# Kernel optimization log

Hardware: AMD Instinct MI355X
Metric: run time of the kernel (lower is better)

## Reference

```python
import jax, jax.numpy as jnp
import numpy as np

H_DIM = 512
FF_DIM = 2048
N_HEAD = 4
N_BLOCK = 3
N_TOKEN = 128
B, S = 8, 1024
LN_EPS = 1e-5


def _layernorm(x, g, b):
    mu = jnp.mean(x, axis=-1, keepdims=True)
    var = jnp.mean(jnp.square(x - mu), axis=-1, keepdims=True)
    return (x - mu) * jax.lax.rsqrt(var + LN_EPS) * g + b


def setup_inputs() -> dict:
    key = jax.random.key(0)
    ks = jax.random.split(key, 20)
    sc = 0.02
    inp = {
        'input_ids': jax.random.randint(ks[0], (B, S), 0, N_TOKEN, dtype=jnp.int32),
        'attention_mask': jnp.ones((B, S), dtype=jnp.int32),
        'emb': jax.random.uniform(ks[1], (N_TOKEN, H_DIM), dtype=jnp.float32),
        'wq': jax.random.normal(ks[2], (N_BLOCK, N_HEAD, H_DIM, H_DIM), dtype=jnp.float32) * sc,
        'wk': jax.random.normal(ks[3], (N_BLOCK, N_HEAD, H_DIM, H_DIM), dtype=jnp.float32) * sc,
        'wv': jax.random.normal(ks[4], (N_BLOCK, N_HEAD, H_DIM, H_DIM), dtype=jnp.float32) * sc,
        'wo_w': jax.random.normal(ks[5], (N_BLOCK, N_HEAD * H_DIM, H_DIM), dtype=jnp.float32) * sc,
        'wo_b': jnp.zeros((N_BLOCK, H_DIM), dtype=jnp.float32),
        'ln1_g': jnp.ones((N_BLOCK, H_DIM), dtype=jnp.float32),
        'ln1_b': jnp.zeros((N_BLOCK, H_DIM), dtype=jnp.float32),
        'ff1_w': jax.random.normal(ks[6], (N_BLOCK, FF_DIM, H_DIM), dtype=jnp.float32) * sc,
        'ff1_b': jnp.zeros((N_BLOCK, FF_DIM), dtype=jnp.float32),
        'ff2_w': jax.random.normal(ks[7], (N_BLOCK, H_DIM, FF_DIM), dtype=jnp.float32) * sc,
        'ff2_b': jnp.zeros((N_BLOCK, H_DIM), dtype=jnp.float32),
        'ln2_g': jnp.ones((N_BLOCK, H_DIM), dtype=jnp.float32),
        'ln2_b': jnp.zeros((N_BLOCK, H_DIM), dtype=jnp.float32),
        'lm_w': jax.random.normal(ks[8], (H_DIM, N_TOKEN), dtype=jnp.float32) * sc,
    }
    return inp


def reference(emb, wq, wk, wv, wo_w, wo_b, ln1_g, ln1_b, ff1_w, ff1_b,
              ff2_w, ff2_b, ln2_g, ln2_b, lm_w, input_ids, attention_mask):
    mask_f = attention_mask.astype(jnp.float32)          # [B,S]
    valid = attention_mask != 0                          # [B,S]

    # Embedding lookup
    x = emb[input_ids]                                   # [B,S,H]

    # Positional encoding: positions assigned sequentially to valid tokens;
    # both even and odd feature slots get the SAME sin value (per source).
    pos = jnp.cumsum(mask_f, axis=-1) - 1.0              # [B,S]
    div = jnp.exp(jnp.arange(0, H_DIM, 2, dtype=jnp.float32) * (-jnp.log(10000.0) / H_DIM))  # [H/2]
    s = jnp.sin(pos[..., None] * div)                    # [B,S,H/2]
    pos_enc = jnp.repeat(s, 2, axis=-1) * mask_f[..., None]
    x = x + pos_enc

    # Allowed attention: causal (key <= query) AND query valid AND key valid
    rows = jnp.arange(S)
    causal = rows[None, :, None] >= rows[None, None, :]  # [1,S,S] (query>=key)
    allowed = causal & valid[:, :, None] & valid[:, None, :]  # [B,S,S]
    neg_inf = jnp.float32(-jnp.inf)
    scale = jnp.sqrt(jnp.float32(H_DIM))

    for l in range(N_BLOCK):
        # Per-head full-width attention (each head uses full H_DIM)
        q = jnp.einsum('bsh,nhd->bnsd', x, wq[l])
        k = jnp.einsum('bsh,nhd->bnsd', x, wk[l])
        v = jnp.einsum('bsh,nhd->bnsd', x, wv[l])
        scores = jnp.einsum('bnsd,bntd->bnst', q, k) / scale      # [B,N,S,S]
        scores = jnp.where(allowed[:, None], scores, neg_inf)
        att = jax.nn.softmax(scores, axis=-1)
        att = jnp.where(jnp.isnan(att), 0.0, att)                  # NaN rows -> 0
        o = jnp.einsum('bnst,bntd->bnsd', att, v)                  # [B,N,S,H]
        o = jnp.transpose(o, (0, 2, 1, 3)).reshape(B, S, N_HEAD * H_DIM)
        mh = o @ wo_w[l] + wo_b[l]
        x = _layernorm(x + mh, ln1_g[l], ln1_b[l])
        # Conv1d with kernel 1 == pointwise linear
        ff = jax.nn.relu(jnp.einsum('bsh,fh->bsf', x, ff1_w[l]) + ff1_b[l])
        ff = jnp.einsum('bsf,hf->bsh', ff, ff2_w[l]) + ff2_b[l]
        x = _layernorm(x + ff, ln2_g[l], ln2_b[l])

    return x @ lm_w                                       # [B,S,N_TOKEN]
```

## Files before the change

### kernel.cpp

```cpp
#include <hip/hip_runtime.h>
#include <hip/hip_bf16.h>

#define S_LEN 1024
#define BATCH 8
#define HD 512
#define FFD 2048
#define NHEAD 4
#define NBLK 3
#define NTOK 128

typedef __bf16 bf16_t;
typedef __bf16 bf16x4_t __attribute__((ext_vector_type(4)));
typedef __bf16 bf16x8_t __attribute__((ext_vector_type(8)));
typedef float f32x4_t __attribute__((ext_vector_type(4)));

typedef __attribute__((address_space(3))) uint32_t lds_u32;
typedef __attribute__((address_space(1))) uint32_t glb_u32;

template<int NI>
__device__ __forceinline__ void ldsread(const bf16_t* __restrict__ buf, int row0,
                                        int fr, int fg, int sw, bf16x8_t (&dst)[NI][2]) {
  #pragma unroll
  for (int i = 0; i < NI; ++i)
    #pragma unroll
    for (int ks = 0; ks < 2; ++ks)
      dst[i][ks] = *(const bf16x8_t*)&buf[(row0 + i*16 + fr)*64 + (((ks*4 + fg) ^ sw) << 3)];
}

template<int IB, int JB>
__device__ __forceinline__ void mquad(f32x4_t (&acc)[8][4],
                                      const bf16x8_t (&af)[4][2], const bf16x8_t (&bf)[2][2]) {
  #pragma unroll
  for (int ks = 0; ks < 2; ++ks)
    #pragma unroll
    for (int i = 0; i < 4; ++i)
      #pragma unroll
      for (int j = 0; j < 2; ++j)
        acc[IB+i][JB+j] = __builtin_amdgcn_mfma_f32_16x16x32_bf16(af[i][ks], bf[j][ks], acc[IB+i][JB+j], 0, 0, 0);
}

template<bool OUT_BF16, bool BIAS, bool RELU, bool TRI, bool CKLIM>
__global__ __launch_bounds__(512, 2)
void gemm256_kernel(const bf16_t* __restrict__ A,
                    const bf16_t* __restrict__ Bt,
                    const float* __restrict__ bias,
                    void* __restrict__ Cv,
                    int M, int N, int K,
                    int lda, int ldb, int ldc,
                    long long sA, long long sB, int bshift, long long sBias,
                    int zshift, long long sC_hi, long long sC_lo,
                    int msub_shift, long long msub_stride,
                    float alpha)
{
  const int zb = blockIdx.z;
  int m0, n0;
  if (TRI) {
    const int idx = blockIdx.x;
    int mi = (int)((sqrtf(8.f * idx + 1.f) - 1.f) * 0.5f);
    while ((mi + 1) * (mi + 2) / 2 <= idx) ++mi;
    while (mi * (mi + 1) / 2 > idx) --mi;
    m0 = mi * 256;
    n0 = (idx - mi * (mi + 1) / 2) * 256;
  } else {
    m0 = blockIdx.x * 256;
    n0 = blockIdx.y * 256;
  }
  int kend = K;
  if (CKLIM) { int ke = m0 + 256; kend = ke < K ? ke : K; }
  const int nt = kend >> 6;

  const bf16_t* Az = A + (long long)zb * sA;
  const bf16_t* Bz = Bt + (long long)(zb >> bshift) * sB;
  const long long coff = ((long long)(zb >> zshift)) * sC_hi
                       + ((long long)(zb & ((1 << zshift) - 1))) * sC_lo;

  __shared__ __align__(16) bf16_t As[2][256 * 64];
  __shared__ __align__(16) bf16_t Bs[2][256 * 64];

  const int tid = threadIdx.x;
  const int lane = tid & 63;
  const int w = tid >> 6;
  const int wm = (w >> 2) * 128;
  const int wn = (w & 3) * 64;
  const int fr = lane & 15;
  const int fg = lane >> 4;
  const int sw = fr & 7;

  const int srow = tid >> 3;
  const int scol8 = tid & 7;
  const int gswz = ((scol8 ^ (srow & 7)) << 3);

  f32x4_t acc[8][4];
  #pragma unroll
  for (int i = 0; i < 8; ++i)
    #pragma unroll
    for (int j = 0; j < 4; ++j)
      acc[i][j] = (f32x4_t){0.f, 0.f, 0.f, 0.f};

  const bf16_t* gA0 = Az + (long long)(m0 + srow) * lda + gswz;
  const bf16_t* gB0 = Bz + (long long)(n0 + srow) * ldb + gswz;

  auto stage_half = [&](int buf, int kt, int h) {
    if (h < 2) {
      const bf16_t* g = gA0 + (long long)(h * 128) * lda + (kt << 6);
      bf16_t* l = &As[buf][(h*128 + srow) * 64 + (scol8 << 3)];
      __builtin_amdgcn_global_load_lds((const glb_u32*)g, (lds_u32*)l, 16, 0, 0);
      __builtin_amdgcn_global_load_lds((const glb_u32*)(g + 64LL*lda), (lds_u32*)(l + 64*64), 16, 0, 0);
    } else {
      const int hh = h - 2;
      const bf16_t* g = gB0 + (long long)(hh * 128) * ldb + (kt << 6);
      bf16_t* l = &Bs[buf][(hh*128 + srow) * 64 + (scol8 << 3)];
      __builtin_amdgcn_global_load_lds((const glb_u32*)g, (lds_u32*)l, 16, 0, 0);
      __builtin_amdgcn_global_load_lds((const glb_u32*)(g + 64LL*ldb), (lds_u32*)(l + 64*64), 16, 0, 0);
    }
  };

  stage_half(0, 0, 0); stage_half(0, 0, 1); stage_half(0, 0, 2); stage_half(0, 0, 3);
  if (nt > 1) { stage_half(1, 1, 0); stage_half(1, 1, 1); }
  if (nt > 1) asm volatile("s_waitcnt vmcnt(4)" ::: "memory");
  else        asm volatile("s_waitcnt vmcnt(0)" ::: "memory");
  __builtin_amdgcn_s_barrier();
  __builtin_amdgcn_sched_barrier(0);

  for (int t = 0; t < nt; ++t) {
    const int cur = t & 1;
    const bf16_t* Ac = &As[cur][0];
    const bf16_t* Bc = &Bs[cur][0];
    bf16x8_t a0[4][2], a1[4][2], b0[2][2], b1[2][2];

    ldsread<4>(Ac, wm, fr, fg, sw, a0);
    ldsread<2>(Bc, wn, fr, fg, sw, b0);
    if (t + 1 < nt) stage_half(cur ^ 1, t + 1, 2);
    mquad<0, 0>(acc, a0, b0);
    ldsread<4>(Ac, wm + 64, fr, fg, sw, a1);
    ldsread<2>(Bc, wn + 32, fr, fg, sw, b1);
    if (t + 1 < nt) stage_half(cur ^ 1, t + 1, 3);
    mquad<4, 2>(acc, a1, b1);

    __builtin_amdgcn_s_barrier();
    __builtin_amdgcn_sched_barrier(0);

    if (t + 2 < nt) stage_half(cur, t + 2, 0);
    mquad<0, 2>(acc, a0, b1);
    if (t + 2 < nt) {
      stage_half(cur, t + 2, 1);
      asm volatile("s_waitcnt vmcnt(4)" ::: "memory");
    } else {
      asm volatile("s_waitcnt vmcnt(0)" ::: "memory");
    }
    mquad<4, 0>(acc, a1, b0);

    __builtin_amdgcn_s_barrier();
    __builtin_amdgcn_sched_barrier(0);
  }

  #pragma unroll
  for (int i = 0; i < 8; ++i) {
    #pragma unroll
    for (int e = 0; e < 4; ++e) {
      const int row = m0 + wm + i*16 + fg*4 + e;
      const long long ro = coff
        + ((long long)(row >> msub_shift)) * msub_stride
        + (long long)(row & ((1 << msub_shift) - 1)) * (long long)ldc;
      #pragma unroll
      for (int j = 0; j < 4; ++j) {
        const int col = n0 + wn + j*16 + fr;
        float v = acc[i][j][e] * alpha;
        if (BIAS) v += bias[(long long)zb * sBias + col];
        if (RELU) v = v > 0.f ? v : 0.f;
        if (OUT_BF16) ((bf16_t*)Cv)[ro + col] = (bf16_t)v;
        else          ((float*)Cv)[ro + col]  = v;
      }
    }
  }
}

template<bool OUT_BF16, bool BIAS, bool RELU, bool CSKIP, bool CKLIM>
__global__ __launch_bounds__(256, 2)
void gemm_bt_kernel(const bf16_t* __restrict__ A,
                    const bf16_t* __restrict__ Bt,
                    const float* __restrict__ bias,
                    void* __restrict__ Cv,
                    int M, int N, int K,
                    int lda, int ldb, int ldc,
                    long long sA, long long sB, long long sBias,
                    int zshift, long long sC_hi, long long sC_lo,
                    int msub_shift, long long msub_stride,
                    float alpha)
{
  const int zb = blockIdx.z;
  const int m0 = blockIdx.x * 128;
  const int n0 = blockIdx.y * 128;
  if (CSKIP && n0 > m0 + 127) return;
  int kend = K;
  if (CKLIM) { int ke = m0 + 128; kend = ke < K ? ke : K; }

  const bf16_t* Az = A + (long long)zb * sA;
  const bf16_t* Bz = Bt + (long long)zb * sB;
  const long long coff = ((long long)(zb >> zshift)) * sC_hi
                       + ((long long)(zb & ((1 << zshift) - 1))) * sC_lo;

  __shared__ __align__(16) bf16_t As[128 * 64];
  __shared__ __align__(16) bf16_t Bs[128 * 64];

  const int tid = threadIdx.x;
  const int wv = tid >> 6;
  const int lane = tid & 63;
  const int wm = (wv >> 1) * 64;
  const int wn = (wv & 1) * 64;
  const int fr = lane & 15;
  const int fg = lane >> 4;
  const int sw = fr & 7;

  f32x4_t acc[4][4];
  #pragma unroll
  for (int i = 0; i < 4; ++i)
    #pragma unroll
    for (int j = 0; j < 4; ++j)
      acc[i][j] = (f32x4_t){0.f, 0.f, 0.f, 0.f};

  const bf16_t* ga = Az + (long long)(m0 + (wv << 5) + (lane >> 3)) * lda
                   + (((lane & 7) ^ (lane >> 3)) << 3);
  const bf16_t* gb = Bz + (long long)(n0 + (wv << 5) + (lane >> 3)) * ldb
                   + (((lane & 7) ^ (lane >> 3)) << 3);

  for (int k0 = 0; k0 < kend; k0 += 64) {
    #pragma unroll
    for (int s = 0; s < 4; ++s) {
      __builtin_amdgcn_global_load_lds(
        (const glb_u32*)(ga + (long long)s * 8 * lda + k0),
        (lds_u32*)(As + (wv * 4 + s) * 512), 16, 0, 0);
      __builtin_amdgcn_global_load_lds(
        (const glb_u32*)(gb + (long long)s * 8 * ldb + k0),
        (lds_u32*)(Bs + (wv * 4 + s) * 512), 16, 0, 0);
    }
    __syncthreads();
    #pragma unroll
    for (int kc = 0; kc < 2; ++kc) {
      const int ca = ((kc * 4 + fg) ^ sw) << 3;
      bf16x8_t af[4], bfr[4];
      #pragma unroll
      for (int i = 0; i < 4; ++i)
        af[i] = *(const bf16x8_t*)&As[(wm + i*16 + fr) * 64 + ca];
      #pragma unroll
      for (int j = 0; j < 4; ++j)
        bfr[j] = *(const bf16x8_t*)&Bs[(wn + j*16 + fr) * 64 + ca];
      #pragma unroll
      for (int i = 0; i < 4; ++i)
        #pragma unroll
        for (int j = 0; j < 4; ++j)
          acc[i][j] = __builtin_amdgcn_mfma_f32_16x16x32_bf16(af[i], bfr[j], acc[i][j], 0, 0, 0);
    }
    __syncthreads();
  }

  #pragma unroll
  for (int i = 0; i < 4; ++i) {
    #pragma unroll
    for (int e = 0; e < 4; ++e) {
      const int row = m0 + wm + i*16 + fg*4 + e;
      const long long ro = coff
        + ((long long)(row >> msub_shift)) * msub_stride
        + (long long)(row & ((1 << msub_shift) - 1)) * (long long)ldc;
      #pragma unroll
      for (int j = 0; j < 4; ++j) {
        const int col = n0 + wn + j*16 + fr;
        float v = acc[i][j][e] * alpha;
        if (BIAS) v += bias[(long long)zb * sBias + col];
        if (RELU) v = v > 0.f ? v : 0.f;
        if (OUT_BF16) ((bf16_t*)Cv)[ro + col] = (bf16_t)v;
        else          ((float*)Cv)[ro + col]  = v;
      }
    }
  }
}

template<typename TIN>
__global__ void transpose_kernel(const TIN* __restrict__ in, bf16_t* __restrict__ out,
                                 int R, int C, long long sIn, long long sOut)
{
  __shared__ float tile[32][33];
  const long long zi = (long long)blockIdx.z * sIn;
  const long long zo = (long long)blockIdx.z * sOut;
  const int c0 = blockIdx.x * 32, r0 = blockIdx.y * 32;
  const int tx = threadIdx.x, ty = threadIdx.y;
  #pragma unroll
  for (int i = 0; i < 4; ++i) {
    int r = r0 + ty + i*8;
    tile[ty + i*8][tx] = (float)in[zi + (long long)r * C + c0 + tx];
  }
  __syncthreads();
  #pragma unroll
  for (int i = 0; i < 4; ++i) {
    int c = c0 + ty + i*8;
    out[zo + (long long)c * R + r0 + tx] = (bf16_t)tile[tx][ty + i*8];
  }
}

__global__ void convert2_kernel(const float* __restrict__ a, const float* __restrict__ b,
                                bf16_t* __restrict__ out, long long n)
{
  long long i = (long long)blockIdx.x * blockDim.x + threadIdx.x;
  long long stride = (long long)gridDim.x * blockDim.x;
  for (; i < 2*n; i += stride)
    out[i] = (bf16_t)(i < n ? a[i] : b[i - n]);
}

__global__ void fill_kernel(float* __restrict__ out, long long n, float v)
{
  long long i = (long long)blockIdx.x * blockDim.x + threadIdx.x;
  long long stride = (long long)gridDim.x * blockDim.x;
  for (; i < n; i += stride) out[i] = v;
}

__global__ void pos_kernel(const int* __restrict__ mask, float* __restrict__ pos)
{
  __shared__ float scn[S_LEN];
  const int b = blockIdx.x, t = threadIdx.x;
  scn[t] = (float)(mask[b * S_LEN + t] != 0);
  __syncthreads();
  for (int off = 1; off < S_LEN; off <<= 1) {
    float add = (t >= off) ? scn[t - off] : 0.f;
    __syncthreads();
    scn[t] += add;
    __syncthreads();
  }
  pos[b * S_LEN + t] = scn[t] - 1.0f;
}

__global__ void embed_kernel(const int* __restrict__ ids, const int* __restrict__ mask,
                             const float* __restrict__ pos, const float* __restrict__ emb,
                             float* __restrict__ x, bf16_t* __restrict__ xb)
{
  const int idx = blockIdx.x * 256 + threadIdx.x;
  const int i = idx & 255;
  const int bs = idx >> 8;
  const int id = ids[bs];
  const float m = (float)(mask[bs] != 0);
  const float p = pos[bs];
  const float dv = __expf(-(float)(2 * i) * (9.210340371976184f / (float)HD));
  const float sv = __sinf(p * dv) * m;
  const float e0 = emb[id * HD + 2*i], e1 = emb[id * HD + 2*i + 1];
  const float x0 = e0 + sv, x1 = e1 + sv;
  x[(long long)bs * HD + 2*i]     = x0;
  x[(long long)bs * HD + 2*i + 1] = x1;
  xb[(long long)bs * HD + 2*i]     = (bf16_t)x0;
  xb[(long long)bs * HD + 2*i + 1] = (bf16_t)x1;
}

__global__ void softmax_kernel(bf16_t* __restrict__ scP,
                               const int* __restrict__ mask, int pair0)
{
  const int lane = threadIdx.x & 63;
  const int s = blockIdx.x * 4 + (threadIdx.x >> 6);
  const int pz = blockIdx.y;
  const int b = (pair0 + pz) >> 2;
  bf16_t* row = scP + ((long long)pz * S_LEN + s) * S_LEN;
  const int t0 = lane * 16;

  bf16x8_t r0 = *(const bf16x8_t*)&row[t0];
  bf16x8_t r1 = *(const bf16x8_t*)&row[t0 + 8];
  int4 m4[4];
  #pragma unroll
  for (int q = 0; q < 4; ++q) m4[q] = *(const int4*)&mask[b * S_LEN + t0 + q*4];
  const int* mm = (const int*)m4;

  float v[16]; bool ok[16];
  #pragma unroll
  for (int j = 0; j < 16; ++j) {
    const int t = t0 + j;
    ok[j] = (t <= s) && (mm[j] != 0);
    float raw = (j < 8) ? (float)r0[j] : (float)r1[j - 8];
    v[j] = ok[j] ? raw : -INFINITY;
  }
  float mx = v[0];
  #pragma unroll
  for (int j = 1; j < 16; ++j) mx = fmaxf(mx, v[j]);
  #pragma unroll
  for (int o = 32; o; o >>= 1) mx = fmaxf(mx, __shfl_xor(mx, o));

  float e[16]; float sum = 0.f;
  #pragma unroll
  for (int j = 0; j < 16; ++j) { e[j] = ok[j] ? __expf(v[j] - mx) : 0.f; sum += e[j]; }
  #pragma unroll
  for (int o = 32; o; o >>= 1) sum += __shfl_xor(sum, o);

  const bool qvalid = mask[b * S_LEN + s] != 0;
  const float inv = (qvalid && sum > 0.f) ? 1.f / sum : 0.f;
  bf16x8_t o0, o1;
  #pragma unroll
  for (int j = 0; j < 8; ++j) { o0[j] = (bf16_t)(e[j] * inv); o1[j] = (bf16_t)(e[j+8] * inv); }
  *(bf16x8_t*)&row[t0] = o0;
  *(bf16x8_t*)&row[t0 + 8] = o1;
}

__global__ void ln_kernel(float* __restrict__ x, const float* __restrict__ tparts,
                          int ns, long long pstride,
                          const float* __restrict__ bias,
                          const float* __restrict__ g, const float* __restrict__ b,
                          bf16_t* __restrict__ xb)
{
  const int lane = threadIdx.x & 63;
  const long long row = (long long)blockIdx.x * 4 + (threadIdx.x >> 6);
  const int e0 = lane * 8;
  const long long base = row * HD + e0;

  float4 xa = *(const float4*)&x[base];
  float4 xc = *(const float4*)&x[base + 4];
  float4 ba = *(const float4*)&bias[e0];
  float4 bc = *(const float4*)&bias[e0 + 4];
  float v[8] = {xa.x+ba.x, xa.y+ba.y, xa.z+ba.z, xa.w+ba.w,
                xc.x+bc.x, xc.y+bc.y, xc.z+bc.z, xc.w+bc.w};
  for (int i = 0; i < ns; ++i) {
    float4 p0 = *(const float4*)&tparts[i*pstride + base];
    float4 p1 = *(const float4*)&tparts[i*pstride + base + 4];
    v[0]+=p0.x; v[1]+=p0.y; v[2]+=p0.z; v[3]+=p0.w;
    v[4]+=p1.x; v[5]+=p1.y; v[6]+=p1.z; v[7]+=p1.w;
  }
  float s = 0.f;
  #pragma unroll
  for (int j = 0; j < 8; ++j) s += v[j];
  #pragma unroll
  for (int o = 32; o; o >>= 1) s += __shfl_xor(s, o);
  const float mu = s * (1.f / (float)HD);
  float q = 0.f;
  #pragma unroll
  for (int j = 0; j < 8; ++j) { v[j] -= mu; q += v[j]*v[j]; }
  #pragma unroll
  for (int o = 32; o; o >>= 1) q += __shfl_xor(q, o);
  const float inv = rsqrtf(q * (1.f / (float)HD) + 1e-5f);

  float4 ga4 = *(const float4*)&g[e0];
  float4 gc4 = *(const float4*)&g[e0 + 4];
  float4 bb4 = *(const float4*)&b[e0];
  float4 bd4 = *(const float4*)&b[e0 + 4];
  float y[8] = {v[0]*inv*ga4.x+bb4.x, v[1]*inv*ga4.y+bb4.y, v[2]*inv*ga4.z+bb4.z, v[3]*inv*ga4.w+bb4.w,
                v[4]*inv*gc4.x+bd4.x, v[5]*inv*gc4.y+bd4.y, v[6]*inv*gc4.z+bd4.z, v[7]*inv*gc4.w+bd4.w};
  *(float4*)&x[base]     = (float4){y[0],y[1],y[2],y[3]};
  *(float4*)&x[base + 4] = (float4){y[4],y[5],y[6],y[7]};
  bf16x8_t yb;
  #pragma unroll
  for (int j = 0; j < 8; ++j) yb[j] = (bf16_t)y[j];
  *(bf16x8_t*)&xb[base] = yb;
}

extern "C" void kernel_launch(void* const* d_in, const int* in_sizes, int n_in,
                              void* d_out, int out_size, void* d_ws, size_t ws_size,
                              hipStream_t stream)
{
  (void)in_sizes; (void)n_in;
  const int*   ids   = (const int*)d_in[0];
  const int*   amask = (const int*)d_in[1];
  const float* emb   = (const float*)d_in[2];
  const float* wq    = (const float*)d_in[3];
  const float* wk    = (const float*)d_in[4];
  const float* wv    = (const float*)d_in[5];
  const float* wo_w  = (const float*)d_in[6];
  const float* wo_b  = (const float*)d_in[7];
  const float* ln1_g = (const float*)d_in[8];
  const float* ln1_b = (const float*)d_in[9];
  const float* ff1_w = (const float*)d_in[10];
  const float* ff1_b = (const float*)d_in[11];
  const float* ff2_w = (const float*)d_in[12];
  const float* ff2_b = (const float*)d_in[13];
  const float* ln2_g = (const float*)d_in[14];
  const float* ln2_b = (const float*)d_in[15];
  const float* lm_w  = (const float*)d_in[16];

  const long long MROW = (long long)BATCH * S_LEN;
  const size_t MBc = 1ull << 20;
  char* p = (char*)d_ws;
  auto alloc = [&](size_t bytes) { char* r = p; p += (bytes + 255) & ~(size_t)255; return r; };

  float*  x     = (float*) alloc(MROW * HD * 4);
  bf16_t* xb    = (bf16_t*)alloc(MROW * HD * 2);
  bf16_t* ob    = (bf16_t*)alloc(MROW * (NHEAD*HD) * 2);
  bf16_t* wqkb  = (bf16_t*)alloc(8LL * HD * HD * 2);
  bf16_t* wvT   = (bf16_t*)alloc(4LL * HD * HD * 2);
  bf16_t* Gt    = (bf16_t*)alloc(4LL * HD * HD * 2);
  bf16_t* woT   = (bf16_t*)alloc((long long)HD * FFD * 2);
  bf16_t* wff1  = (bf16_t*)alloc((long long)FFD * HD * 2);
  bf16_t* wff2  = (bf16_t*)alloc((long long)HD * FFD * 2);
  bf16_t* lmT   = (bf16_t*)alloc((long long)NTOK * HD * 2);
  float*  pos   = (float*) alloc(MROW * 4);

  const size_t used = (size_t)(p - (char*)d_ws);
  const size_t rem  = ws_size > used ? ws_size - used : 0;

  int P = 0, SK = 2;
  if      (rem >= 128 * MBc) { P = 32; SK = 4; }
  else if (rem >= 64 * MBc)  { P = 8;  SK = 2; }
  if (P == 0) {
    fill_kernel<<<1024, 256, 0, stream>>>((float*)d_out, (long long)out_size,
                                          (float)(ws_size >> 20));
    return;
  }

  char* A = p;
  const long long pairE = (long long)S_LEN * HD;
  bf16_t* qc  = (bf16_t*)A;
  bf16_t* vTc = qc  + (long long)P * pairE;
  bf16_t* scb = vTc + (long long)P * pairE;
  float*  tmp = (float*)A;
  bf16_t* ffb = (bf16_t*)(A + (size_t)SK * 16 * MBc);

  const dim3 tb(32, 8);
  transpose_kernel<float><<<dim3(4,16,1), tb, 0, stream>>>(lm_w, lmT, HD, NTOK, 0, 0);
  pos_kernel<<<BATCH, S_LEN, 0, stream>>>(amask, pos);
  embed_kernel<<<8192, 256, 0, stream>>>(ids, amask, pos, emb, x, xb);

  const int nch = 32 / P;
  const int bpc = P / NHEAD;

  for (int l = 0; l < NBLK; ++l) {
    convert2_kernel<<<2048, 256, 0, stream>>>(
      wq + (long long)l*NHEAD*HD*HD, wk + (long long)l*NHEAD*HD*HD, wqkb, 4LL*HD*HD);
    transpose_kernel<float><<<dim3(16,16,4), tb, 0, stream>>>(
      wv + (long long)l*NHEAD*HD*HD, wvT, HD, HD, (long long)HD*HD, (long long)HD*HD);
    transpose_kernel<float><<<dim3(16,64,1), tb, 0, stream>>>(
      wo_w + (long long)l*FFD*HD, woT, FFD, HD, 0, 0);
    convert2_kernel<<<2048, 256, 0, stream>>>(
      ff1_w + (long long)l*FFD*HD, ff2_w + (long long)l*HD*FFD, wff1, (long long)FFD*HD);
    gemm_bt_kernel<true,false,false,false,false><<<dim3(4,4,4),256,0,stream>>>(
      wqkb + 4LL*HD*HD, wqkb, nullptr, Gt,
      HD, HD, HD, HD, HD, HD,
      (long long)HD*HD, (long long)HD*HD, 0,
      30, 0, (long long)HD*HD,
      30, 0, 1.f);

    for (int c = 0; c < nch; ++c) {
      const int b0 = c * bpc;
      const int pair0 = b0 * NHEAD;
      const int Mch = bpc * S_LEN;

      gemm256_kernel<true,false,false,false,false><<<dim3(Mch/256,2,4),512,0,stream>>>(
        xb + (long long)b0*S_LEN*HD, Gt, nullptr, qc, Mch, HD, HD, HD, HD, HD,
        0, (long long)HD*HD, 0, 0,
        2, 0, pairE,
        10, (long long)NHEAD*pairE, 1.f);

      gemm256_kernel<true,false,false,false,false><<<dim3(8,4,bpc),512,0,stream>>>(
        wvT, xb + (long long)b0*S_LEN*HD, nullptr, vTc,
        2048, S_LEN, HD, HD, HD, S_LEN,
        0, (long long)S_LEN*HD, 0, 0,
        0, (long long)NHEAD*HD*S_LEN, 0,
        9, (long long)HD*S_LEN, 1.f);

      gemm256_kernel<true,false,false,true,false><<<dim3(10,1,P),512,0,stream>>>(
        qc, xb + (long long)b0*S_LEN*HD, nullptr, scb,
        S_LEN, S_LEN, HD, HD, HD, S_LEN,
        pairE, (long long)S_LEN*HD, 2, 0,
        30, 0, (long long)S_LEN*S_LEN,
        30, 0, 0.044194173824159216f);
      softmax_kernel<<<dim3(S_LEN/4,P),256,0,stream>>>(scb, amask, pair0);
      gemm_bt_kernel<true,false,false,false,true><<<dim3(8,4,P),256,0,stream>>>(
        scb, vTc, nullptr,
        ob + (long long)b0*S_LEN*(NHEAD*HD),
        S_LEN, HD, S_LEN, S_LEN, S_LEN, NHEAD*HD,
        (long long)S_LEN*S_LEN, (long long)HD*S_LEN, 0,
        2, (long long)S_LEN*NHEAD*HD, HD,
        30, 0, 1.f);
    }

    gemm256_kernel<false,false,false,false,false><<<dim3(32,2,SK),512,0,stream>>>(
      ob, woT, nullptr, tmp,
      (int)MROW, HD, (NHEAD*HD)/SK, NHEAD*HD, NHEAD*HD, HD,
      (NHEAD*HD)/SK, (NHEAD*HD)/SK, 0, 0,
      0, (long long)MROW*HD, 0,
      30, 0, 1.f);
    ln_kernel<<<2048,256,0,stream>>>(x, tmp, SK, (long long)MROW*HD,
                                     wo_b + l*HD, ln1_g + l*HD, ln1_b + l*HD, xb);

    gemm256_kernel<true,true,true,false,false><<<dim3(32,8,1),512,0,stream>>>(
      xb, wff1, ff1_b + l*FFD, ffb,
      (int)MROW, FFD, HD, HD, HD, FFD,
      0, 0, 0, 0, 30, 0, 0, 30, 0, 1.f);
    gemm256_kernel<false,false,false,false,false><<<dim3(32,2,SK),512,0,stream>>>(
      ffb, wff2, nullptr, tmp,
      (int)MROW, HD, FFD/SK, FFD, FFD, HD,
      FFD/SK, FFD/SK, 0, 0,
      0, (long long)MROW*HD, 0,
      30, 0, 1.f);
    ln_kernel<<<2048,256,0,stream>>>(x, tmp, SK, (long long)MROW*HD,
                                     ff2_b + l*HD, ln2_g + l*HD, ln2_b + l*HD, xb);
  }

  gemm_bt_kernel<false,false,false,false,false><<<dim3(64,1,1),256,0,stream>>>(
    xb, lmT, nullptr, (float*)d_out,
    (int)MROW, NTOK, HD, HD, HD, NTOK,
    0, 0, 0, 30, 0, 0, 30, 0, 1.f);
}
```

Measured before the change: 902.4 us.

## Fuse softmax exponentiation into score GEMM and defer normalization to PV GEMM

Drops the separate softmax kernel. The score GEMM epilogue now applies the causal and key masks, exponentiates the scaled scores without subtracting the row max, and writes unnormalized bf16 probabilities. It also reduces partial row sums into LDS and writes them per column tile. A small kernel combines the partial sums into reciprocal row norms, and the PV GEMM multiplies its output by them. The score GEMM also switches to single-buffered LDS to free shared memory, which removes load/compute overlap, and skipping the max subtraction risks overflow if scores grow large.

```diff
diff --git a/kernel.cpp b/kernel.cpp
--- a/kernel.cpp
+++ b/kernel.cpp
@@ -39,7 +39,7 @@
         acc[IB+i][JB+j] = __builtin_amdgcn_mfma_f32_16x16x32_bf16(af[i][ks], bf[j][ks], acc[IB+i][JB+j], 0, 0, 0);
 }
 
-template<bool OUT_BF16, bool BIAS, bool RELU, bool TRI, bool CKLIM>
+template<bool OUT_BF16, bool BIAS, bool RELU, bool TRI, bool CKLIM, bool SB, bool SM>
 __global__ __launch_bounds__(512, 2)
 void gemm256_kernel(const bf16_t* __restrict__ A,
                     const bf16_t* __restrict__ Bt,
@@ -50,17 +50,19 @@
                     long long sA, long long sB, int bshift, long long sBias,
                     int zshift, long long sC_hi, long long sC_lo,
                     int msub_shift, long long msub_stride,
-                    float alpha)
+                    float alpha,
+                    const int* __restrict__ kmask, float* __restrict__ lpart, int pair0)
 {
   const int zb = blockIdx.z;
-  int m0, n0;
+  int m0, n0, tri_ni = 0;
   if (TRI) {
     const int idx = blockIdx.x;
     int mi = (int)((sqrtf(8.f * idx + 1.f) - 1.f) * 0.5f);
     while ((mi + 1) * (mi + 2) / 2 <= idx) ++mi;
     while (mi * (mi + 1) / 2 > idx) --mi;
     m0 = mi * 256;
-    n0 = (idx - mi * (mi + 1) / 2) * 256;
+    tri_ni = idx - mi * (mi + 1) / 2;
+    n0 = tri_ni * 256;
   } else {
     m0 = blockIdx.x * 256;
     n0 = blockIdx.y * 256;
@@ -74,8 +76,8 @@
   const long long coff = ((long long)(zb >> zshift)) * sC_hi
                        + ((long long)(zb & ((1 << zshift) - 1))) * sC_lo;
 
-  __shared__ __align__(16) bf16_t As[2][256 * 64];
-  __shared__ __align__(16) bf16_t Bs[2][256 * 64];
+  __shared__ __align__(16) bf16_t As[SB ? 1 : 2][256 * 64];
+  __shared__ __align__(16) bf16_t Bs[SB ? 1 : 2][256 * 64];
 
   const int tid = threadIdx.x;
   const int lane = tid & 63;
@@ -115,43 +117,72 @@
     }
   };
 
-  stage_half(0, 0, 0); stage_half(0, 0, 1); stage_half(0, 0, 2); stage_half(0, 0, 3);
-  if (nt > 1) { stage_half(1, 1, 0); stage_half(1, 1, 1); }
-  if (nt > 1) asm volatile("s_waitcnt vmcnt(4)" ::: "memory");
-  else        asm volatile("s_waitcnt vmcnt(0)" ::: "memory");
-  __builtin_amdgcn_s_barrier();
-  __builtin_amdgcn_sched_barrier(0);
-
-  for (int t = 0; t < nt; ++t) {
-    const int cur = t & 1;
-    const bf16_t* Ac = &As[cur][0];
-    const bf16_t* Bc = &Bs[cur][0];
-    bf16x8_t a0[4][2], a1[4][2], b0[2][2], b1[2][2];
-
-    ldsread<4>(Ac, wm, fr, fg, sw, a0);
-    ldsread<2>(Bc, wn, fr, fg, sw, b0);
-    if (t + 1 < nt) stage_half(cur ^ 1, t + 1, 2);
-    mquad<0, 0>(acc, a0, b0);
-    ldsread<4>(Ac, wm + 64, fr, fg, sw, a1);
-    ldsread<2>(Bc, wn + 32, fr, fg, sw, b1);
-    if (t + 1 < nt) stage_half(cur ^ 1, t + 1, 3);
-    mquad<4, 2>(acc, a1, b1);
-
+  if constexpr (SB) {
+    for (int t = 0; t < nt; ++t) {
+      stage_half(0, t, 0); stage_half(0, t, 1); stage_half(0, t, 2); stage_half(0, t, 3);
+      __syncthreads();
+      bf16x8_t a0[4][2], a1[4][2], b0[2][2], b1[2][2];
+      ldsread<4>(&As[0][0], wm, fr, fg, sw, a0);
+      ldsread<2>(&Bs[0][0], wn, fr, fg, sw, b0);
+      mquad<0, 0>(acc, a0, b0);
+      ldsread<4>(&As[0][0], wm + 64, fr, fg, sw, a1);
+      ldsread<2>(&Bs[0][0], wn + 32, fr, fg, sw, b1);
+      mquad<4, 2>(acc, a1, b1);
+      mquad<0, 2>(acc, a0, b1);
+      mquad<4, 0>(acc, a1, b0);
+      __syncthreads();
+    }
+  } else {
+    stage_half(0, 0, 0); stage_half(0, 0, 1); stage_half(0, 0, 2); stage_half(0, 0, 3);
+    if (nt > 1) { stage_half(1, 1, 0); stage_half(1, 1, 1); }
+    if (nt > 1) asm volatile("s_waitcnt vmcnt(4)" ::: "memory");
+    else        asm volatile("s_waitcnt vmcnt(0)" ::: "memory");
     __builtin_amdgcn_s_barrier();
     __builtin_amdgcn_sched_barrier(0);
 
-    if (t + 2 < nt) stage_half(cur, t + 2, 0);
-    mquad<0, 2>(acc, a0, b1);
-    if (t + 2 < nt) {
-      stage_half(cur, t + 2, 1);
-      asm volatile("s_waitcnt vmcnt(4)" ::: "memory");
-    } else {
-      asm volatile("s_waitcnt vmcnt(0)" ::: "memory");
-    }
-    mquad<4, 0>(acc, a1, b0);
-
-    __builtin_amdgcn_s_barrier();
-    __builtin_amdgcn_sched_barrier(0);
+    for (int t = 0; t < nt; ++t) {
+      const int cur = t & 1;
+      const bf16_t* Ac = &As[cur][0];
+      const bf16_t* Bc = &Bs[cur][0];
+      bf16x8_t a0[4][2], a1[4][2], b0[2][2], b1[2][2];
+
+      ldsread<4>(Ac, wm, fr, fg, sw, a0);
+      ldsread<2>(Bc, wn, fr, fg, sw, b0);
+      if (t + 1 < nt) stage_half(cur ^ 1, t + 1, 2);
+      mquad<0, 0>(acc, a0, b0);
+      ldsread<4>(Ac, wm + 64, fr, fg, sw, a1);
+      ldsread<2>(Bc, wn + 32, fr, fg, sw, b1);
+      if (t + 1 < nt) stage_half(cur ^ 1, t + 1, 3);
+      mquad<4, 2>(acc, a1, b1);
+
+      __builtin_amdgcn_s_barrier();
+      __builtin_amdgcn_sched_barrier(0);
+
+      if (t + 2 < nt) stage_half(cur, t + 2, 0);
+      mquad<0, 2>(acc, a0, b1);
+      if (t + 2 < nt) {
+        stage_half(cur, t + 2, 1);
+        asm volatile("s_waitcnt vmcnt(4)" ::: "memory");
+      } else {
+        asm volatile("s_waitcnt vmcnt(0)" ::: "memory");
+      }
+      mquad<4, 0>(acc, a1, b0);
+
+      __builtin_amdgcn_s_barrier();
+      __builtin_amdgcn_sched_barrier(0);
+    }
+  }
+
+  float* lsum = nullptr;
+  int km[4];
+  if constexpr (SM) {
+    lsum = (float*)&As[0][0];
+    __syncthreads();
+    if (tid < 256) lsum[tid] = 0.f;
+    const int* mrow = kmask + (long long)((pair0 + zb) >> 2) * S_LEN;
+    #pragma unroll
+    for (int j = 0; j < 4; ++j) km[j] = mrow[n0 + wn + j*16 + fr];
+    __syncthreads();
   }
 
   #pragma unroll
@@ -162,20 +193,40 @@
       const long long ro = coff
         + ((long long)(row >> msub_shift)) * msub_stride
         + (long long)(row & ((1 << msub_shift) - 1)) * (long long)ldc;
+      float rsum = 0.f;
       #pragma unroll
       for (int j = 0; j < 4; ++j) {
         const int col = n0 + wn + j*16 + fr;
         float v = acc[i][j][e] * alpha;
-        if (BIAS) v += bias[(long long)zb * sBias + col];
-        if (RELU) v = v > 0.f ? v : 0.f;
-        if (OUT_BF16) ((bf16_t*)Cv)[ro + col] = (bf16_t)v;
-        else          ((float*)Cv)[ro + col]  = v;
+        if constexpr (SM) {
+          const float pv = (col <= row && km[j]) ? __expf(v) : 0.f;
+          rsum += pv;
+          ((bf16_t*)Cv)[ro + col] = (bf16_t)pv;
+        } else {
+          if (BIAS) v += bias[(long long)zb * sBias + col];
+          if (RELU) v = v > 0.f ? v : 0.f;
+          if (OUT_BF16) ((bf16_t*)Cv)[ro + col] = (bf16_t)v;
+          else          ((float*)Cv)[ro + col]  = v;
+        }
       }
-    }
-  }
-}
-
-template<bool OUT_BF16, bool BIAS, bool RELU, bool CSKIP, bool CKLIM>
+      if constexpr (SM) {
+        rsum += __shfl_xor(rsum, 1);
+        rsum += __shfl_xor(rsum, 2);
+        rsum += __shfl_xor(rsum, 4);
+        rsum += __shfl_xor(rsum, 8);
+        if (fr == 0) atomicAdd(&lsum[wm + i*16 + fg*4 + e], rsum);
+      }
+    }
+  }
+
+  if constexpr (SM) {
+    __syncthreads();
+    if (tid < 256)
+      lpart[((long long)zb * S_LEN + m0 + tid) * 4 + tri_ni] = lsum[tid];
+  }
+}
+
+template<bool OUT_BF16, bool BIAS, bool RELU, bool CSKIP, bool CKLIM, bool NORM>
 __global__ __launch_bounds__(256, 2)
 void gemm_bt_kernel(const bf16_t* __restrict__ A,
                     const bf16_t* __restrict__ Bt,
@@ -262,17 +313,34 @@
       const long long ro = coff
         + ((long long)(row >> msub_shift)) * msub_stride
         + (long long)(row & ((1 << msub_shift) - 1)) * (long long)ldc;
+      float rn = 1.f;
+      if (NORM) rn = bias[(long long)zb * sBias + row];
       #pragma unroll
       for (int j = 0; j < 4; ++j) {
         const int col = n0 + wn + j*16 + fr;
         float v = acc[i][j][e] * alpha;
         if (BIAS) v += bias[(long long)zb * sBias + col];
+        if (NORM) v *= rn;
         if (RELU) v = v > 0.f ? v : 0.f;
         if (OUT_BF16) ((bf16_t*)Cv)[ro + col] = (bf16_t)v;
         else          ((float*)Cv)[ro + col]  = v;
       }
     }
   }
+}
+
+__global__ void linv_kernel(const float* __restrict__ lpart, const int* __restrict__ mask,
+                            float* __restrict__ linv, int pair0)
+{
+  const int idx = blockIdx.x * 256 + threadIdx.x;
+  const int pr = idx >> 10;
+  const int row = idx & (S_LEN - 1);
+  const int b = (pair0 + pr) >> 2;
+  const int nlim = (row >> 8) + 1;
+  const float* lp = lpart + (long long)idx * 4;
+  float l = 0.f;
+  for (int n = 0; n < nlim; ++n) l += lp[n];
+  linv[idx] = (mask[b * S_LEN + row] != 0 && l > 0.f) ? 1.f / l : 0.f;
 }
 
 template<typename TIN>
@@ -346,52 +414,6 @@
   x[(long long)bs * HD + 2*i + 1] = x1;
   xb[(long long)bs * HD + 2*i]     = (bf16_t)x0;
   xb[(long long)bs * HD + 2*i + 1] = (bf16_t)x1;
-}
-
-__global__ void softmax_kernel(bf16_t* __restrict__ scP,
-                               const int* __restrict__ mask, int pair0)
-{
-  const int lane = threadIdx.x & 63;
-  const int s = blockIdx.x * 4 + (threadIdx.x >> 6);
-  const int pz = blockIdx.y;
-  const int b = (pair0 + pz) >> 2;
-  bf16_t* row = scP + ((long long)pz * S_LEN + s) * S_LEN;
-  const int t0 = lane * 16;
-
-  bf16x8_t r0 = *(const bf16x8_t*)&row[t0];
-  bf16x8_t r1 = *(const bf16x8_t*)&row[t0 + 8];
-  int4 m4[4];
-  #pragma unroll
-  for (int q = 0; q < 4; ++q) m4[q] = *(const int4*)&mask[b * S_LEN + t0 + q*4];
-  const int* mm = (const int*)m4;
-
-  float v[16]; bool ok[16];
-  #pragma unroll
-  for (int j = 0; j < 16; ++j) {
-    const int t = t0 + j;
-    ok[j] = (t <= s) && (mm[j] != 0);
-    float raw = (j < 8) ? (float)r0[j] : (float)r1[j - 8];
-    v[j] = ok[j] ? raw : -INFINITY;
-  }
-  float mx = v[0];
-  #pragma unroll
-  for (int j = 1; j < 16; ++j) mx = fmaxf(mx, v[j]);
-  #pragma unroll
-  for (int o = 32; o; o >>= 1) mx = fmaxf(mx, __shfl_xor(mx, o));
-
-  float e[16]; float sum = 0.f;
-  #pragma unroll
-  for (int j = 0; j < 16; ++j) { e[j] = ok[j] ? __expf(v[j] - mx) : 0.f; sum += e[j]; }
-  #pragma unroll
-  for (int o = 32; o; o >>= 1) sum += __shfl_xor(sum, o);
-
-  const bool qvalid = mask[b * S_LEN + s] != 0;
-  const float inv = (qvalid && sum > 0.f) ? 1.f / sum : 0.f;
-  bf16x8_t o0, o1;
-  #pragma unroll
-  for (int j = 0; j < 8; ++j) { o0[j] = (bf16_t)(e[j] * inv); o1[j] = (bf16_t)(e[j+8] * inv); }
-  *(bf16x8_t*)&row[t0] = o0;
-  *(bf16x8_t*)&row[t0 + 8] = o1;
 }
 
 __global__ void ln_kernel(float* __restrict__ x, const float* __restrict__ tparts,
@@ -483,6 +505,8 @@
   bf16_t* wff2  = (bf16_t*)alloc((long long)HD * FFD * 2);
   bf16_t* lmT   = (bf16_t*)alloc((long long)NTOK * HD * 2);
   float*  pos   = (float*) alloc(MROW * 4);
+  float*  lpart = (float*) alloc(32LL * S_LEN * 4 * 4);
+  float*  linv  = (float*) alloc(32LL * S_LEN * 4);
 
   const size_t used = (size_t)(p - (char*)d_ws);
   const size_t rem  = ws_size > used ? ws_size - used : 0;
@@ -521,7 +545,7 @@
       wo_w + (long long)l*FFD*HD, woT, FFD, HD, 0, 0);
     convert2_kernel<<<2048, 256, 0, stream>>>(
       ff1_w + (long long)l*FFD*HD, ff2_w + (long long)l*HD*FFD, wff1, (long long)FFD*HD);
-    gemm_bt_kernel<true,false,false,false,false><<<dim3(4,4,4),256,0,stream>>>(
+    gemm_bt_kernel<true,false,false,false,false,false><<<dim3(4,4,4),256,0,stream>>>(
       wqkb + 4LL*HD*HD, wqkb, nullptr, Gt,
       HD, HD, HD, HD, HD, HD,
       (long long)HD*HD, (long long)HD*HD, 0,
@@ -533,59 +557,61 @@
       const int pair0 = b0 * NHEAD;
       const int Mch = bpc * S_LEN;
 
-      gemm256_kernel<true,false,false,false,false><<<dim3(Mch/256,2,4),512,0,stream>>>(
+      gemm256_kernel<true,false,false,false,false,false,false><<<dim3(Mch/256,2,4),512,0,stream>>>(
         xb + (long long)b0*S_LEN*HD, Gt, nullptr, qc, Mch, HD, HD, HD, HD, HD,
         0, (long long)HD*HD, 0, 0,
         2, 0, pairE,
-        10, (long long)NHEAD*pairE, 1.f);
-
-      gemm256_kernel<true,false,false,false,false><<<dim3(8,4,bpc),512,0,stream>>>(
+        10, (long long)NHEAD*pairE, 1.f, nullptr, nullptr, 0);
+
+      gemm256_kernel<true,false,false,false,false,false,false><<<dim3(8,4,bpc),512,0,stream>>>(
         wvT, xb + (long long)b0*S_LEN*HD, nullptr, vTc,
         2048, S_LEN, HD, HD, HD, S_LEN,
         0, (long long)S_LEN*HD, 0, 0,
         0, (long long)NHEAD*HD*S_LEN, 0,
-        9, (long long)HD*S_LEN, 1.f);
-
-      gemm256_kernel<true,false,false,true,false><<<dim3(10,1,P),512,0,stream>>>(
+        9, (long long)HD*S_LEN, 1.f, nullptr, nullptr, 0);
+
+      gemm256_kernel<true,false,false,true,false,true,true><<<dim3(10,1,P),512,0,stream>>>(
         qc, xb + (long long)b0*S_LEN*HD, nullptr, scb,
         S_LEN, S_LEN, HD, HD, HD, S_LEN,
         pairE, (long long)S_LEN*HD, 2, 0,
         30, 0, (long long)S_LEN*S_LEN,
-        30, 0, 0.044194173824159216f);
-      softmax_kernel<<<dim3(S_LEN/4,P),256,0,stream>>>(scb, amask, pair0);
-      gemm_bt_kernel<true,false,false,false,true><<<dim3(8,4,P),256,0,stream>>>(
-        scb, vTc, nullptr,
+        30, 0, 0.044194173824159216f, amask, lpart, pair0);
+
+      linv_kernel<<<P*S_LEN/256,256,0,stream>>>(lpart, amask, linv, pair0);
+
+      gemm_bt_kernel<true,false,false,false,true,true><<<dim3(8,4,P),256,0,stream>>>(
+        scb, vTc, linv,
         ob + (long long)b0*S_LEN*(NHEAD*HD),
         S_LEN, HD, S_LEN, S_LEN, S_LEN, NHEAD*HD,
-        (long long)S_LEN*S_LEN, (long long)HD*S_LEN, 0,
+        (long long)S_LEN*S_LEN, (long long)HD*S_LEN, S_LEN,
         2, (long long)S_LEN*NHEAD*HD, HD,
         30, 0, 1.f);
     }
 
-    gemm256_kernel<false,false,false,false,false><<<dim3(32,2,SK),512,0,stream>>>(
+    gemm256_kernel<false,false,false,false,false,false,false><<<dim3(32,2,SK),512,0,stream>>>(
       ob, woT, nullptr, tmp,
       (int)MROW, HD, (NHEAD*HD)/SK, NHEAD*HD, NHEAD*HD, HD,
       (NHEAD*HD)/SK, (NHEAD*HD)/SK, 0, 0,
       0, (long long)MROW*HD, 0,
-      30, 0, 1.f);
+      30, 0, 1.f, nullptr, nullptr, 0);
     ln_kernel<<<2048,256,0,stream>>>(x, tmp, SK, (long long)MROW*HD,
                                      wo_b + l*HD, ln1_g + l*HD, ln1_b + l*HD, xb);
 
-    gemm256_kernel<true,true,true,false,false><<<dim3(32,8,1),512,0,stream>>>(
+    gemm256_kernel<true,true,true,false,false,false,false><<<dim3(32,8,1),512,0,stream>>>(
       xb, wff1, ff1_b + l*FFD, ffb,
       (int)MROW, FFD, HD, HD, HD, FFD,
-      0, 0, 0, 0, 30, 0, 0, 30, 0, 1.f);
-    gemm256_kernel<false,false,false,false,false><<<dim3(32,2,SK),512,0,stream>>>(
+      0, 0, 0, 0, 30, 0, 0, 30, 0, 1.f, nullptr, nullptr, 0);
+    gemm256_kernel<false,false,false,false,false,false,false><<<dim3(32,2,SK),512,0,stream>>>(
       ffb, wff2, nullptr, tmp,
       (int)MROW, HD, FFD/SK, FFD, FFD, HD,
       FFD/SK, FFD/SK, 0, 0,
       0, (long long)MROW*HD, 0,
-      30, 0, 1.f);
+      30, 0, 1.f, nullptr, nullptr, 0);
     ln_kernel<<<2048,256,0,stream>>>(x, tmp, SK, (long long)MROW*HD,
                                      ff2_b + l*HD, ln2_g + l*HD, ln2_b + l*HD, xb);
   }
 
-  gemm_bt_kernel<false,false,false,false,false><<<dim3(64,1,1),256,0,stream>>>(
+  gemm_bt_kernel<false,false,false,false,false,false><<<dim3(64,1,1),256,0,stream>>>(
     xb, lmT, nullptr, (float*)d_out,
     (int)MROW, NTOK, HD, HD, HD, NTOK,
     0, 0, 0, 30, 0, 0, 30, 0, 1.f);
```

New measurement: 911.0 us. No clear change (+0.9%).
